# Optimization experiments

Hardware: AMD Instinct MI355X
Metric: run time of the kernel (lower is better)

The kernel has to match this reference:

```python
import jax, jax.numpy as jnp
import numpy as np

N, D, DIN, S, R = 128, 2560, 5120, 16, 160  # users, d_model, d_inner, d_state, dt_rank


def setup_inputs() -> dict:
    key = jax.random.key(0)
    ks = jax.random.split(key, 16)
    f = lambda k, shape, s: jax.random.normal(k, shape, dtype=jnp.float32) * s
    return {
        "x": f(ks[0], (1, 1, N, D), 1.0),
        "conv_state0": f(ks[1], (1, 1, N, DIN), 0.1),
        "conv_state1": f(ks[2], (1, 1, N, DIN), 0.1),
        "conv_state2": f(ks[3], (1, 1, N, DIN), 0.1),
        "conv_state3": f(ks[4], (1, 1, N, DIN), 0.1),
        "ssm_state": f(ks[5], (N, DIN, S), 0.1),
        "ssm_proj": f(ks[6], (D, DIN), 0.02),
        "mlp_proj": f(ks[7], (D, DIN), 0.02),
        "down_proj": f(ks[8], (DIN, D), 0.02),
        "conv_w": f(ks[9], (4, DIN), 0.2),
        "conv_bias": f(ks[10], (DIN,), 0.1),
        "x_proj_w": f(ks[11], (DIN, R + 2 * S), 0.02),
        "dt_proj_w": f(ks[12], (R, DIN), 0.05),
        "dt_proj_b": f(ks[13], (DIN,), 0.1),
        "A_log": jnp.log(jnp.broadcast_to(jnp.arange(1, S + 1, dtype=jnp.float32), (DIN, S))),
        "D_param": jnp.ones((DIN,), jnp.float32),
    }


def reference(x, conv_state0, conv_state1, conv_state2, conv_state3, ssm_state,
              ssm_proj, mlp_proj, down_proj, conv_w, conv_bias,
              x_proj_w, dt_proj_w, dt_proj_b, A_log, D_param):
    r = dt_proj_w.shape[0]
    s = A_log.shape[1]
    x2 = x[0, 0]                         # (N, D)
    xs = x2 @ ssm_proj                   # (N, DIN) in_proj (ssm half)
    # shifted conv state window: oldest state (conv_state0) is dropped
    states = (conv_state1[0, 0], conv_state2[0, 0], conv_state3[0, 0], xs)
    conv_out = conv_bias + conv_w[0] * states[0] + conv_w[1] * states[1] \
        + conv_w[2] * states[2] + conv_w[3] * states[3]   # (N, DIN)
    u = jax.nn.silu(conv_out)
    # selective-scan single step (TtMambaSSM)
    proj = u @ x_proj_w                  # (N, R + 2S)
    dt = jax.nn.softplus(proj[:, :r] @ dt_proj_w + dt_proj_b)  # (N, DIN)
    Bm = proj[:, r:r + s]                # (N, S)
    Cm = proj[:, r + s:]                 # (N, S)
    A = -jnp.exp(A_log)                  # (DIN, S)
    dA = jnp.exp(dt[:, :, None] * A[None])                     # (N, DIN, S)
    h = dA * ssm_state + dt[:, :, None] * Bm[:, None, :] * u[:, :, None]
    y = jnp.einsum('nds,ns->nd', h, Cm) + D_param * u          # (N, DIN)
    # residual/gate branch and output projection (note: no silu on res, as in source)
    res = x2 @ mlp_proj                  # (N, DIN)
    out = (y * res) @ down_proj          # (N, D)
    return out[None, None]               # (1, 1, N, D)
```

## Files before the change

kernel.cpp:

```cpp
#include <hip/hip_runtime.h>

using u16 = unsigned short;
using u32 = unsigned int;

typedef __attribute__((ext_vector_type(8))) short short8;
typedef __attribute__((ext_vector_type(4))) float floatx4;

constexpr int TOKENS = 128;
constexpr int DM = 2560;
constexpr int DI = 5120;
constexpr int NS = 16;
constexpr int NR = 160;
constexpr int NP = 192;

constexpr size_t XS_OFF   = 0;
constexpr size_t RES_OFF  = XS_OFF  + (size_t)TOKENS * DI;
constexpr size_t U_OFF    = RES_OFF + (size_t)TOKENS * DI;
constexpr size_t DT_OFF   = U_OFF   + (size_t)TOKENS * DI;
constexpr size_t PROJ_OFF = DT_OFF  + (size_t)TOKENS * DI;
constexpr size_t OACC_OFF = PROJ_OFF + (size_t)TOKENS * NP;

__device__ __forceinline__ float bf2f(u16 h) {
  u32 u = ((u32)h) << 16;
  return __builtin_bit_cast(float, u);
}
__device__ __forceinline__ u16 f2bf(float f) {
  u32 u = __builtin_bit_cast(u32, f);
  u += 0x7FFFu + ((u >> 16) & 1u);
  return (u16)(u >> 16);
}
__device__ __forceinline__ u32 pk2(float a, float b) {
  return (u32)f2bf(a) | ((u32)f2bf(b) << 16);
}
__device__ __forceinline__ float ldsc(const void* p, size_t i, bool bf) {
  return bf ? bf2f(((const u16*)p)[i]) : ((const float*)p)[i];
}
__device__ __forceinline__ uint4 ld8(const void* p, size_t i, bool bf) {
  if (bf) return *(const uint4*)((const u16*)p + i);
  const float4* f = (const float4*)((const float*)p + i);
  float4 a = f[0], b = f[1];
  return (uint4){pk2(a.x, a.y), pk2(a.z, a.w), pk2(b.x, b.y), pk2(b.z, b.w)};
}
__device__ __forceinline__ void ld8f(const void* p, size_t i, bool bf, float* o) {
  if (bf) {
    uint4 v = *(const uint4*)((const u16*)p + i);
    const u16* h = (const u16*)&v;
#pragma unroll
    for (int e = 0; e < 8; e++) o[e] = bf2f(h[e]);
  } else {
    const float4* f = (const float4*)((const float*)p + i);
    float4 a = f[0], b = f[1];
    o[0] = a.x; o[1] = a.y; o[2] = a.z; o[3] = a.w;
    o[4] = b.x; o[5] = b.y; o[6] = b.z; o[7] = b.w;
  }
}

struct GemmP {
  const void* A; int lda; int a_ws;
  const void* B; const void* B2;
  float* C; float* C2;
  int ldb; int ldc;
  int ksteps;
  int nx_half;
  int atomic;
  const u32* probe;
};

template <int BK>
__global__ __launch_bounds__(256, 4) void gemm_t(GemmP p) {
  constexpr int NBLK = BK / 8;
  constexpr int MASK = NBLK - 1;
  constexpr int KK = BK / 32;
  constexpr int LOGN = (BK == 64) ? 3 : 2;
  constexpr int RP = 256 / NBLK;
  constexpr int PA = 128 / RP;

  __shared__ __align__(16) u16 As[128 * BK];
  __shared__ __align__(16) u16 Bs[64 * BK];

  const bool bf = (p.probe[0] != 0u);
  const int tid = threadIdx.x;
  const int bx = blockIdx.x;
  const void* B = p.B; float* C = p.C;
  int nblk = bx;
  if (bx >= p.nx_half) { B = p.B2; C = p.C2; nblk = bx - p.nx_half; }
  const int n0 = nblk * 64;
  const int kstart = blockIdx.y * p.ksteps * BK;

  const int wave = tid >> 6, lane = tid & 63;
  const int q = lane >> 4, l16 = lane & 15;
  const int wx = wave & 1, wy = wave >> 1;

  const bool a_f32 = p.a_ws || !bf;

  const int ac = tid & MASK;
  const int am0 = tid >> LOGN;
  const int bc = tid & 7;
  const int br = tid >> 3;
  const int bn8 = bc * 8;

  floatx4 acc[4][2];
#pragma unroll
  for (int mi = 0; mi < 4; mi++)
#pragma unroll
    for (int ni = 0; ni < 2; ni++) acc[mi][ni] = (floatx4){0.f, 0.f, 0.f, 0.f};

  uint4 aR[PA];
  uint4 bR[KK];

  auto load_tiles = [&](int ks) {
    const int kb = kstart + ks * BK;
#pragma unroll
    for (int pa = 0; pa < PA; pa++) {
      const int m = am0 + pa * RP;
      const size_t off = (size_t)m * p.lda + kb + ac * 8;
      if (!a_f32) {
        aR[pa] = *(const uint4*)((const u16*)p.A + off);
      } else {
        const float4* f = (const float4*)((const float*)p.A + off);
        float4 x0 = f[0], x1 = f[1];
        aR[pa] = (uint4){pk2(x0.x, x0.y), pk2(x0.z, x0.w),
                         pk2(x1.x, x1.y), pk2(x1.z, x1.w)};
      }
    }
    if constexpr (BK == 64) {
      bR[0] = ld8(B, (size_t)(kb + 2 * br) * p.ldb + n0 + bn8, bf);
      bR[1] = ld8(B, (size_t)(kb + 2 * br + 1) * p.ldb + n0 + bn8, bf);
    } else {
      bR[0] = ld8(B, (size_t)(kb + br) * p.ldb + n0 + bn8, bf);
    }
  };

  auto store_tiles = [&]() {
#pragma unroll
    for (int pa = 0; pa < PA; pa++) {
      const int m = am0 + pa * RP;
      *(uint4*)&As[m * BK + ((ac ^ (m & MASK)) << 3)] = aR[pa];
    }
    if constexpr (BK == 64) {
      const u16* lo = (const u16*)&bR[0];
      const u16* hi = (const u16*)&bR[1];
      const int k2 = 2 * br;
#pragma unroll
      for (int j = 0; j < 8; j++) {
        const int n = bn8 + j;
        const int blk = (k2 >> 3) ^ ((n ^ (n >> 3)) & MASK);
        *(u32*)&Bs[n * BK + (blk << 3) + (k2 & 7)] =
            (u32)lo[j] | ((u32)hi[j] << 16);
      }
    } else {
      const u16* lo = (const u16*)&bR[0];
#pragma unroll
      for (int j = 0; j < 8; j++) {
        const int n = bn8 + j;
        const int blk = (br >> 3) ^ ((n ^ (n >> 3)) & MASK);
        Bs[n * BK + (blk << 3) + (br & 7)] = lo[j];
      }
    }
  };

  const int swA = l16 & MASK;
  const int arow = (wy * 64 + l16) * BK;
  int nrow[2], swb[2];
#pragma unroll
  for (int ni = 0; ni < 2; ni++) {
    const int n = wx * 32 + ni * 16 + l16;
    nrow[ni] = n * BK;
    swb[ni] = (n ^ (n >> 3)) & MASK;
  }

  load_tiles(0);

  for (int ks = 0;;) {
    __syncthreads();
    store_tiles();
    __syncthreads();
    const bool more = (ks + 1 < p.ksteps);
    if (more) load_tiles(ks + 1);

#pragma unroll
    for (int kk = 0; kk < KK; kk++) {
      const int kq = kk * 4 + q;
      const int ao = (kq ^ swA) << 3;
      short8 a[4];
#pragma unroll
      for (int mi = 0; mi < 4; mi++)
        a[mi] = __builtin_bit_cast(short8,
            *(const uint4*)&As[arow + mi * 16 * BK + ao]);
      short8 b[2];
#pragma unroll
      for (int ni = 0; ni < 2; ni++)
        b[ni] = __builtin_bit_cast(short8,
            *(const uint4*)&Bs[nrow[ni] + ((kq ^ swb[ni]) << 3)]);
#pragma unroll
      for (int mi = 0; mi < 4; mi++)
#pragma unroll
        for (int ni = 0; ni < 2; ni++)
          acc[mi][ni] = __builtin_amdgcn_mfma_f32_16x16x32_bf16(
              a[mi], b[ni], acc[mi][ni], 0, 0, 0);
    }

    if (!more) break;
    ks++;
  }

  if (p.atomic) {
#pragma unroll
    for (int ni = 0; ni < 2; ni++) {
      const int col = n0 + wx * 32 + ni * 16 + l16;
#pragma unroll
      for (int mi = 0; mi < 4; mi++) {
        floatx4 v = acc[mi][ni];
#pragma unroll
        for (int r = 0; r < 4; r++) {
          const int row = wy * 64 + mi * 16 + q * 4 + r;
          atomicAdd(&C[(size_t)row * p.ldc + col], v[r]);
        }
      }
    }
  } else {
#pragma unroll
    for (int ni = 0; ni < 2; ni++) {
      const int col = n0 + wx * 32 + ni * 16 + l16;
#pragma unroll
      for (int mi = 0; mi < 4; mi++) {
        floatx4 v = acc[mi][ni];
#pragma unroll
        for (int r = 0; r < 4; r++) {
          const int row = wy * 64 + mi * 16 + q * 4 + r;
          C[(size_t)row * p.ldc + col] = v[r];
        }
      }
    }
  }
}

__global__ __launch_bounds__(256) void epi_u_k(
    const float* __restrict__ xs_acc, const void* __restrict__ cs1,
    const void* __restrict__ cs2, const void* __restrict__ cs3,
    const void* __restrict__ cw, const void* __restrict__ cb,
    float* __restrict__ u, const u32* __restrict__ probe) {
  const bool bf = (probe[0] != 0u);
  const int idx = blockIdx.x * 256 + threadIdx.x;
  const int n = idx / (DI / 8);
  const int d0 = (idx - n * (DI / 8)) * 8;
  const size_t nd = (size_t)n * DI + d0;
  float xv[8];
  {
    const float4* f = (const float4*)(xs_acc + nd);
    float4 a = f[0], b = f[1];
    xv[0] = a.x; xv[1] = a.y; xv[2] = a.z; xv[3] = a.w;
    xv[4] = b.x; xv[5] = b.y; xv[6] = b.z; xv[7] = b.w;
  }
  float c1[8], c2[8], c3[8], w0[8], w1[8], w2[8], w3[8], bb[8];
  ld8f(cs1, nd, bf, c1);
  ld8f(cs2, nd, bf, c2);
  ld8f(cs3, nd, bf, c3);
  ld8f(cw, (size_t)0 * DI + d0, bf, w0);
  ld8f(cw, (size_t)1 * DI + d0, bf, w1);
  ld8f(cw, (size_t)2 * DI + d0, bf, w2);
  ld8f(cw, (size_t)3 * DI + d0, bf, w3);
  ld8f(cb, d0, bf, bb);
  float o[8];
#pragma unroll
  for (int e = 0; e < 8; e++) {
    float cv = bb[e] + w0[e] * c1[e] + w1[e] * c2[e] + w2[e] * c3[e] +
               w3[e] * xv[e];
    o[e] = cv / (1.0f + __expf(-cv));
  }
  float4* uo = (float4*)(u + nd);
  uo[0] = (float4){o[0], o[1], o[2], o[3]};
  uo[1] = (float4){o[4], o[5], o[6], o[7]};
}

__global__ __launch_bounds__(256) void ssm_k(
    const void* __restrict__ sstate, const void* __restrict__ alog,
    const void* __restrict__ dparam, const void* __restrict__ dtb,
    const float* __restrict__ proj, const float* __restrict__ dtacc,
    const float* __restrict__ u, const float* __restrict__ res,
    float* __restrict__ z, const u32* __restrict__ probe) {
  const bool bf = (probe[0] != 0u);
  const int n = blockIdx.y;
  const int d = blockIdx.x * 256 + threadIdx.x;
  __shared__ float Bsh[NS], Csh[NS];
  if (threadIdx.x < NS)
    Bsh[threadIdx.x] = proj[(size_t)n * NP + NR + threadIdx.x];
  else if (threadIdx.x < 2 * NS)
    Csh[threadIdx.x - NS] = proj[(size_t)n * NP + NR + threadIdx.x];
  __syncthreads();
  const size_t nd = (size_t)n * DI + d;
  const float uv = u[nd], rv = res[nd];
  float sv = dtacc[nd] + ldsc(dtb, d, bf);
  const float dtv = (sv > 20.0f) ? sv : log1pf(__expf(sv));

  float stf[16], alf[16];
  if (bf) {
    u16 st[16], al[16];
    const uint4* sp = (const uint4*)((const u16*)sstate + nd * 16);
    *(uint4*)&st[0] = sp[0]; *(uint4*)&st[8] = sp[1];
    const uint4* ap = (const uint4*)((const u16*)alog + (size_t)d * 16);
    *(uint4*)&al[0] = ap[0]; *(uint4*)&al[8] = ap[1];
#pragma unroll
    for (int s = 0; s < 16; s++) { stf[s] = bf2f(st[s]); alf[s] = bf2f(al[s]); }
  } else {
    const float4* sp = (const float4*)((const float*)sstate + nd * 16);
    const float4* ap = (const float4*)((const float*)alog + (size_t)d * 16);
#pragma unroll
    for (int i = 0; i < 4; i++) {
      float4 s4 = sp[i], a4 = ap[i];
      stf[i * 4 + 0] = s4.x; stf[i * 4 + 1] = s4.y; stf[i * 4 + 2] = s4.z; stf[i * 4 + 3] = s4.w;
      alf[i * 4 + 0] = a4.x; alf[i * 4 + 1] = a4.y; alf[i * 4 + 2] = a4.z; alf[i * 4 + 3] = a4.w;
    }
  }
  float y = 0.f;
#pragma unroll
  for (int s = 0; s < 16; s++) {
    float Aa = -__expf(alf[s]);
    float dA = __expf(dtv * Aa);
    float h = dA * stf[s] + dtv * Bsh[s] * uv;
    y += h * Csh[s];
  }
  y += ldsc(dparam, d, bf) * uv;
  z[nd] = y * rv;
}

__global__ __launch_bounds__(256) void cvt_k(const float* __restrict__ in,
                                             void* __restrict__ out, int n,
                                             const u32* __restrict__ probe) {
  const bool bf = (probe[0] != 0u);
  const int i0 = (blockIdx.x * 256 + threadIdx.x) * 8;
  if (i0 + 8 <= n) {
    const float4* f = (const float4*)(in + i0);
    float4 a = f[0], b = f[1];
    if (bf) {
      uint4 v = {pk2(a.x, a.y), pk2(a.z, a.w), pk2(b.x, b.y), pk2(b.z, b.w)};
      *(uint4*)((u16*)out + i0) = v;
    } else {
      float4* o = (float4*)((float*)out + i0);
      o[0] = a; o[1] = b;
    }
  } else {
    for (int i = i0; i < n; i++) {
      if (bf) ((u16*)out)[i] = f2bf(in[i]);
      else    ((float*)out)[i] = in[i];
    }
  }
}

extern "C" void kernel_launch(void* const* d_in, const int* in_sizes, int n_in,
                              void* d_out, int out_size, void* d_ws, size_t ws_size,
                              hipStream_t stream) {
  const void* x         = d_in[0];
  const void* cs1       = d_in[2];
  const void* cs2       = d_in[3];
  const void* cs3       = d_in[4];
  const void* ssm_state = d_in[5];
  const void* ssm_proj  = d_in[6];
  const void* mlp_proj  = d_in[7];
  const void* down_proj = d_in[8];
  const void* conv_w    = d_in[9];
  const void* conv_b    = d_in[10];
  const void* x_proj_w  = d_in[11];
  const void* dt_proj_w = d_in[12];
  const void* dt_proj_b = d_in[13];
  const void* A_log     = d_in[14];
  const void* D_param   = d_in[15];
  const u32*  probe     = (const u32*)A_log;

  float* ws     = (float*)d_ws;
  float* xs_acc = ws + XS_OFF;
  float* z      = ws + XS_OFF;
  float* res    = ws + RES_OFF;
  float* u      = ws + U_OFF;
  float* dtacc  = ws + DT_OFF;
  float* proj   = ws + PROJ_OFF;
  float* oacc   = ws + OACC_OFF;

  hipMemsetAsync(xs_acc, 0, (size_t)TOKENS * DI * sizeof(float), stream);
  hipMemsetAsync(res,    0, (size_t)TOKENS * DI * sizeof(float), stream);
  hipMemsetAsync(proj,   0, (size_t)TOKENS * NP * sizeof(float), stream);
  hipMemsetAsync(oacc,   0, (size_t)TOKENS * DM * sizeof(float), stream);

  {
    GemmP p{};
    p.A = x; p.lda = DM; p.a_ws = 0;
    p.B = ssm_proj; p.B2 = mlp_proj;
    p.C = xs_acc; p.C2 = res;
    p.ldb = DI; p.ldc = DI;
    p.ksteps = 20; p.nx_half = 80; p.atomic = 1;
    p.probe = probe;
    gemm_t<64><<<dim3(160, 2), 256, 0, stream>>>(p);
  }
  epi_u_k<<<dim3(TOKENS * DI / 8 / 256), 256, 0, stream>>>(
      xs_acc, cs1, cs2, cs3, conv_w, conv_b, u, probe);
  {
    GemmP p{};
    p.A = u; p.lda = DI; p.a_ws = 1;
    p.B = x_proj_w; p.B2 = nullptr;
    p.C = proj; p.C2 = nullptr;
    p.ldb = NP; p.ldc = NP;
    p.ksteps = 4; p.nx_half = 1 << 30; p.atomic = 1;
    p.probe = probe;
    gemm_t<64><<<dim3(3, 20), 256, 0, stream>>>(p);
  }
  {
    GemmP p{};
    p.A = proj; p.lda = NP; p.a_ws = 1;
    p.B = dt_proj_w; p.B2 = nullptr;
    p.C = dtacc; p.C2 = nullptr;
    p.ldb = DI; p.ldc = DI;
    p.ksteps = 5; p.nx_half = 1 << 30; p.atomic = 0;
    p.probe = probe;
    gemm_t<32><<<dim3(DI / 64, 1), 256, 0, stream>>>(p);
  }
  ssm_k<<<dim3(DI / 256, TOKENS), 256, 0, stream>>>(
      ssm_state, A_log, D_param, dt_proj_b, proj, dtacc, u, res, z, probe);
  {
    GemmP p{};
    p.A = z; p.lda = DI; p.a_ws = 1;
    p.B = down_proj; p.B2 = nullptr;
    p.C = oacc; p.C2 = nullptr;
    p.ldb = DM; p.ldc = DM;
    p.ksteps = 20; p.nx_half = 1 << 30; p.atomic = 1;
    p.probe = probe;
    gemm_t<64><<<dim3(DM / 64, 4), 256, 0, stream>>>(p);
  }
  cvt_k<<<dim3((out_size / 8 + 255) / 256), 256, 0, stream>>>(oacc, d_out, out_size, probe);
}
```

Measured before the change: 389.4 us.

## Double-buffer GEMM register prefetch, raise split-K, use hardware bf16 pack

The GEMM main loop now keeps two register sets and prefetches tiles two k-steps ahead, so global loads overlap more compute. Every GEMM launch uses a larger split-K factor (4-5x more blocks, fewer k-steps each), and the dt_proj GEMM switches to atomic accumulation into a zeroed buffer. Float-to-bf16 packing uses the v_cvt_pk_bf16_f32 instruction instead of software rounding. The cost is more atomics, an extra memset and higher register pressure.

```diff
diff --git a/kernel.cpp b/kernel.cpp
--- a/kernel.cpp
+++ b/kernel.cpp
@@ -30,7 +30,9 @@
   return (u16)(u >> 16);
 }
 __device__ __forceinline__ u32 pk2(float a, float b) {
-  return (u32)f2bf(a) | ((u32)f2bf(b) << 16);
+  u32 r;
+  asm("v_cvt_pk_bf16_f32 %0, %1, %2" : "=v"(r) : "v"(a), "v"(b));
+  return r;
 }
 __device__ __forceinline__ float ldsc(const void* p, size_t i, bool bf) {
   return bf ? bf2f(((const u16*)p)[i]) : ((const float*)p)[i];
@@ -105,41 +107,38 @@
 #pragma unroll
     for (int ni = 0; ni < 2; ni++) acc[mi][ni] = (floatx4){0.f, 0.f, 0.f, 0.f};
 
-  uint4 aR[PA];
-  uint4 bR[KK];
-
-  auto load_tiles = [&](int ks) {
+  auto load_tiles = [&](int ks, uint4* aO, uint4* bO) {
     const int kb = kstart + ks * BK;
 #pragma unroll
     for (int pa = 0; pa < PA; pa++) {
       const int m = am0 + pa * RP;
       const size_t off = (size_t)m * p.lda + kb + ac * 8;
       if (!a_f32) {
-        aR[pa] = *(const uint4*)((const u16*)p.A + off);
+        aO[pa] = *(const uint4*)((const u16*)p.A + off);
       } else {
         const float4* f = (const float4*)((const float*)p.A + off);
         float4 x0 = f[0], x1 = f[1];
-        aR[pa] = (uint4){pk2(x0.x, x0.y), pk2(x0.z, x0.w),
+        aO[pa] = (uint4){pk2(x0.x, x0.y), pk2(x0.z, x0.w),
                          pk2(x1.x, x1.y), pk2(x1.z, x1.w)};
       }
     }
     if constexpr (BK == 64) {
-      bR[0] = ld8(B, (size_t)(kb + 2 * br) * p.ldb + n0 + bn8, bf);
-      bR[1] = ld8(B, (size_t)(kb + 2 * br + 1) * p.ldb + n0 + bn8, bf);
+      bO[0] = ld8(B, (size_t)(kb + 2 * br) * p.ldb + n0 + bn8, bf);
+      bO[1] = ld8(B, (size_t)(kb + 2 * br + 1) * p.ldb + n0 + bn8, bf);
     } else {
-      bR[0] = ld8(B, (size_t)(kb + br) * p.ldb + n0 + bn8, bf);
+      bO[0] = ld8(B, (size_t)(kb + br) * p.ldb + n0 + bn8, bf);
     }
   };
 
-  auto store_tiles = [&]() {
+  auto store_tiles = [&](const uint4* aO, const uint4* bO) {
 #pragma unroll
     for (int pa = 0; pa < PA; pa++) {
       const int m = am0 + pa * RP;
-      *(uint4*)&As[m * BK + ((ac ^ (m & MASK)) << 3)] = aR[pa];
+      *(uint4*)&As[m * BK + ((ac ^ (m & MASK)) << 3)] = aO[pa];
     }
     if constexpr (BK == 64) {
-      const u16* lo = (const u16*)&bR[0];
-      const u16* hi = (const u16*)&bR[1];
+      const u16* lo = (const u16*)&bO[0];
+      const u16* hi = (const u16*)&bO[1];
       const int k2 = 2 * br;
 #pragma unroll
       for (int j = 0; j < 8; j++) {
@@ -149,7 +148,7 @@
             (u32)lo[j] | ((u32)hi[j] << 16);
       }
     } else {
-      const u16* lo = (const u16*)&bR[0];
+      const u16* lo = (const u16*)&bO[0];
 #pragma unroll
       for (int j = 0; j < 8; j++) {
         const int n = bn8 + j;
@@ -169,15 +168,7 @@
     swb[ni] = (n ^ (n >> 3)) & MASK;
   }
 
-  load_tiles(0);
-
-  for (int ks = 0;;) {
-    __syncthreads();
-    store_tiles();
-    __syncthreads();
-    const bool more = (ks + 1 < p.ksteps);
-    if (more) load_tiles(ks + 1);
-
+  auto compute = [&]() {
 #pragma unroll
     for (int kk = 0; kk < KK; kk++) {
       const int kq = kk * 4 + q;
@@ -199,9 +190,26 @@
           acc[mi][ni] = __builtin_amdgcn_mfma_f32_16x16x32_bf16(
               a[mi], b[ni], acc[mi][ni], 0, 0, 0);
     }
-
-    if (!more) break;
-    ks++;
+  };
+
+  uint4 a0[PA], b0[KK], a1[PA], b1[KK];
+  load_tiles(0, a0, b0);
+  if (p.ksteps > 1) load_tiles(1, a1, b1);
+  int ks = 0;
+  for (;;) {
+    __syncthreads();
+    store_tiles(a0, b0);
+    if (ks + 2 < p.ksteps) load_tiles(ks + 2, a0, b0);
+    __syncthreads();
+    compute();
+    if (++ks == p.ksteps) break;
+
+    __syncthreads();
+    store_tiles(a1, b1);
+    if (ks + 2 < p.ksteps) load_tiles(ks + 2, a1, b1);
+    __syncthreads();
+    compute();
+    if (++ks == p.ksteps) break;
   }
 
   if (p.atomic) {
@@ -378,6 +386,7 @@
 
   hipMemsetAsync(xs_acc, 0, (size_t)TOKENS * DI * sizeof(float), stream);
   hipMemsetAsync(res,    0, (size_t)TOKENS * DI * sizeof(float), stream);
+  hipMemsetAsync(dtacc,  0, (size_t)TOKENS * DI * sizeof(float), stream);
   hipMemsetAsync(proj,   0, (size_t)TOKENS * NP * sizeof(float), stream);
   hipMemsetAsync(oacc,   0, (size_t)TOKENS * DM * sizeof(float), stream);
 
@@ -387,9 +396,9 @@
     p.B = ssm_proj; p.B2 = mlp_proj;
     p.C = xs_acc; p.C2 = res;
     p.ldb = DI; p.ldc = DI;
-    p.ksteps = 20; p.nx_half = 80; p.atomic = 1;
+    p.ksteps = 5; p.nx_half = 80; p.atomic = 1;
     p.probe = probe;
-    gemm_t<64><<<dim3(160, 2), 256, 0, stream>>>(p);
+    gemm_t<64><<<dim3(160, 8), 256, 0, stream>>>(p);
   }
   epi_u_k<<<dim3(TOKENS * DI / 8 / 256), 256, 0, stream>>>(
       xs_acc, cs1, cs2, cs3, conv_w, conv_b, u, probe);
@@ -399,9 +408,9 @@
     p.B = x_proj_w; p.B2 = nullptr;
     p.C = proj; p.C2 = nullptr;
     p.ldb = NP; p.ldc = NP;
-    p.ksteps = 4; p.nx_half = 1 << 30; p.atomic = 1;
+    p.ksteps = 1; p.nx_half = 1 << 30; p.atomic = 1;
     p.probe = probe;
-    gemm_t<64><<<dim3(3, 20), 256, 0, stream>>>(p);
+    gemm_t<64><<<dim3(3, 80), 256, 0, stream>>>(p);
   }
   {
     GemmP p{};
@@ -409,9 +418,9 @@
     p.B = dt_proj_w; p.B2 = nullptr;
     p.C = dtacc; p.C2 = nullptr;
     p.ldb = DI; p.ldc = DI;
-    p.ksteps = 5; p.nx_half = 1 << 30; p.atomic = 0;
+    p.ksteps = 1; p.nx_half = 1 << 30; p.atomic = 1;
     p.probe = probe;
-    gemm_t<32><<<dim3(DI / 64, 1), 256, 0, stream>>>(p);
+    gemm_t<32><<<dim3(DI / 64, 5), 256, 0, stream>>>(p);
   }
   ssm_k<<<dim3(DI / 256, TOKENS), 256, 0, stream>>>(
       ssm_state, A_log, D_param, dt_proj_b, proj, dtacc, u, res, z, probe);
@@ -421,9 +430,9 @@
     p.B = down_proj; p.B2 = nullptr;
     p.C = oacc; p.C2 = nullptr;
     p.ldb = DM; p.ldc = DM;
-    p.ksteps = 20; p.nx_half = 1 << 30; p.atomic = 1;
+    p.ksteps = 5; p.nx_half = 1 << 30; p.atomic = 1;
     p.probe = probe;
-    gemm_t<64><<<dim3(DM / 64, 4), 256, 0, stream>>>(p);
+    gemm_t<64><<<dim3(DM / 64, 16), 256, 0, stream>>>(p);
   }
   cvt_k<<<dim3((out_size / 8 + 255) / 256), 256, 0, stream>>>(oacc, d_out, out_size, probe);
 }
```

Measured after the change: 336.0 us. 1.16x faster.
